# Kernel tuning notes

Hardware: AMD Instinct MI355X
Metric: run time of the kernel (lower is better)

The kernel has to match this reference:

```python
import jax, jax.numpy as jnp
import numpy as np

T, N, D, R, E = 512, 32, 300, 3, 64
NUM_NODES, VG = 70000, 40000


def setup_inputs() -> dict:
    key = jax.random.key(0)
    ks = jax.random.split(key, 10)
    return {
        "x_indices": jax.random.randint(ks[0], (T, N), 0, NUM_NODES),
        "edge_src": jax.random.randint(ks[1], (T, R, E), 0, N),
        "edge_dst": jax.random.randint(ks[2], (T, R, E), 0, N),
        "X": jax.random.normal(ks[3], (NUM_NODES, D), dtype=jnp.float32) * 0.1,
        "conv_W": jax.random.normal(ks[4], (R, D, D), dtype=jnp.float32) * 0.05,
        "W0": jax.random.normal(ks[5], (D, D), dtype=jnp.float32) * 0.05,
        "Wu": jax.random.normal(ks[6], (N * D, D), dtype=jnp.float32) * 0.01,
        "Uu": jax.random.normal(ks[7], (D, D), dtype=jnp.float32) * 0.05,
        "Wg": jax.random.normal(ks[8], (VG, D), dtype=jnp.float32) * 0.05,
        "bg": jnp.zeros((VG,), dtype=jnp.float32),
    }


def gcn_conv(x, W, src, dst):
    """torch_geometric GCNConv(bias=False): add self-loops, D^-1/2 (A+I) D^-1/2 (x W)."""
    n = x.shape[0]
    h = x @ W  # [N, D]
    loop = jnp.arange(n)
    s = jnp.concatenate([src, loop])
    t = jnp.concatenate([dst, loop])
    deg = jax.ops.segment_sum(jnp.ones_like(t, dtype=x.dtype), t, num_segments=n)
    dinv = jnp.where(deg > 0, jax.lax.rsqrt(jnp.maximum(deg, 1e-12)), 0.0)
    norm = dinv[s] * dinv[t]  # [E+N]
    return jax.ops.segment_sum(h[s] * norm[:, None], t, num_segments=n)


def reference(x_indices, edge_src, edge_dst, X, conv_W, W0, Wu, Uu, Wg, bg):
    def step(mem, inp):
        idx, src, dst = inp  # [N], [R,E], [R,E]
        x = X[idx]  # grapharea features [N, D]
        # sum of per-relation GCNConv outputs
        conv = jnp.sum(
            jax.vmap(gcn_conv, in_axes=(None, 0, 0, 0))(x, conv_W, src, dst), axis=0
        )
        proposed = conv + x @ W0  # eye(N) @ (x @ W0) == x @ W0
        # GRU-style update gate: [1, N*D] @ [N*D, D] + mem_row0 @ [D, D]
        gate = jax.nn.sigmoid(x.reshape(1, -1) @ Wu + mem[0:1] @ Uu)  # [1, D]
        new_mem = gate * proposed + (1.0 - gate) * mem  # broadcast over N rows
        logits = jnp.maximum(new_mem[0], 0.0) @ Wg.T + bg  # [VG]
        # memory is a non-grad buffer in torch (.data.copy_): stop gradient through time
        return jax.lax.stop_gradient(new_mem), jax.nn.log_softmax(logits)

    mem0 = jnp.zeros((N, D), dtype=X.dtype)
    _, log_probs = jax.lax.scan(step, mem0, (x_indices, edge_src, edge_dst))
    # include_senses=False: per-step torch.tensor(0) stacked -> zeros([T])
    return log_probs, jnp.zeros((x_indices.shape[0],), dtype=jnp.int32)
```

## Files before the change

kernel.cpp:

```cpp
#include <hip/hip_runtime.h>
#include <hip/hip_bf16.h>
#include <math.h>

#define T_ 512
#define N_ 32
#define D_ 300
#define R_ 3
#define E_ 64
#define VG_ 40000

typedef __attribute__((ext_vector_type(8))) short bf16x8;
typedef __attribute__((ext_vector_type(4))) float f32x4;

#define LGKM_BARRIER() asm volatile("s_waitcnt lgkmcnt(0)\n\ts_barrier" ::: "memory")

static __device__ inline unsigned short f2b(float f) {
  __hip_bfloat16 h = __float2bfloat16(f);
  return *(unsigned short*)&h;
}

__global__ void k_zero(float* __restrict__ p, int n) {
  int i = blockIdx.x * blockDim.x + threadIdx.x;
  if (i < n) p[i] = 0.f;
}

__global__ void k_tr_wu(const float* __restrict__ Wu, unsigned short* __restrict__ Wt) {
  __shared__ float s[32][33];
  int kb = blockIdx.x * 32, nb = blockIdx.y * 32;
  int tn = threadIdx.x & 31, tr = threadIdx.x >> 5;
  for (int i = tr; i < 32; i += 8) {
    int k = kb + i, n = nb + tn;
    s[i][tn] = (n < 300) ? Wu[(size_t)k * 300 + n] : 0.f;
  }
  __syncthreads();
  for (int i = tr; i < 32; i += 8) {
    int n = nb + i, k = kb + tn;
    Wt[(size_t)n * 9600 + k] = f2b(s[tn][i]);
  }
}

__global__ void k_tr_wcat(const float* __restrict__ convW, const float* __restrict__ W0,
                          unsigned short* __restrict__ Wt) {
  __shared__ float s[32][33];
  int kb = blockIdx.x * 32, nb = blockIdx.y * 32;
  int tn = threadIdx.x & 31, tr = threadIdx.x >> 5;
  for (int i = tr; i < 32; i += 8) {
    int k = kb + i, n = nb + tn;
    float v = 0.f;
    if (n < 300 && k < 1200)
      v = (k < 900) ? convW[(size_t)k * 300 + n] : W0[(size_t)(k - 900) * 300 + n];
    s[i][tn] = v;
  }
  __syncthreads();
  for (int i = tr; i < 32; i += 8) {
    int n = nb + i, k = kb + tn;
    Wt[(size_t)n * 1216 + k] = f2b(s[tn][i]);
  }
}

__global__ void k_gather(const int* __restrict__ xidx, const int* __restrict__ esrc,
                         const int* __restrict__ edst, const float* __restrict__ X,
                         unsigned short* __restrict__ xg, unsigned short* __restrict__ Ag)
{
  const int t = blockIdx.x;
  __shared__ int s_idx[N_];
  __shared__ int s_src[R_][E_];
  __shared__ int s_dst[R_][E_];
  __shared__ int s_deg[R_][N_];
  __shared__ float s_dinv[R_][N_];
  const int tid = threadIdx.x;

  if (tid < N_) s_idx[tid] = xidx[t * N_ + tid];
  if (tid < R_ * E_) {
    int r = tid / E_, e = tid % E_;
    s_src[r][e] = esrc[(t * R_ + r) * E_ + e];
    s_dst[r][e] = edst[(t * R_ + r) * E_ + e];
  }
  if (tid < R_ * N_) ((int*)s_deg)[tid] = 1;
  __syncthreads();
  if (tid < R_ * E_) {
    int r = tid / E_;
    atomicAdd(&s_deg[r][s_dst[r][tid % E_]], 1);
  }
  __syncthreads();
  if (tid < R_ * N_) ((float*)s_dinv)[tid] = rsqrtf((float)((int*)s_deg)[tid]);
  __syncthreads();

  for (int nd = tid; nd < N_ * D_; nd += blockDim.x) {
    int n = nd / D_, d = nd % D_;
    xg[(size_t)t * (N_ * D_) + nd] = f2b(X[(size_t)s_idx[n] * D_ + d]);
  }
  if (tid < D_) {
    int d = tid;
    float x0 = X[(size_t)s_idx[0] * D_ + d];
    #pragma unroll
    for (int r = 0; r < R_; ++r) {
      float dinv0 = s_dinv[r][0];
      float acc = dinv0 * dinv0 * x0;
      for (int e = 0; e < E_; ++e) {
        if (s_dst[r][e] == 0) {
          int s = s_src[r][e];
          acc += s_dinv[r][s] * dinv0 * X[(size_t)s_idx[s] * D_ + d];
        }
      }
      Ag[(size_t)t * 1216 + r * D_ + d] = f2b(acc);
    }
    Ag[(size_t)t * 1216 + 900 + d] = f2b(x0);
  }
  if (tid < 16) Ag[(size_t)t * 1216 + 1200 + tid] = 0;
}

template<bool ATOMIC>
__global__ __launch_bounds__(256) void k_bgemm(
    const unsigned short* __restrict__ A,
    const unsigned short* __restrict__ B,
    float* __restrict__ C, int ldc, int Ncols, int K, int kchunk)
{
  const int tid = threadIdx.x;
  const int wid = tid >> 6, lane = tid & 63;
  const int l16 = lane & 15, lq = lane >> 4;
  const int bm = blockIdx.x * 128 + (wid & 1) * 64;
  const int bn = blockIdx.y * 128 + (wid >> 1) * 64;
  const int k0 = blockIdx.z * kchunk;
  const int nk = kchunk / 32;

  f32x4 acc[4][4] = {};
  const unsigned short* ap[4];
  const unsigned short* bp[4];
  #pragma unroll
  for (int mt = 0; mt < 4; ++mt) ap[mt] = A + (size_t)(bm + mt * 16 + l16) * K + k0 + lq * 8;
  #pragma unroll
  for (int nt = 0; nt < 4; ++nt) bp[nt] = B + (size_t)(bn + nt * 16 + l16) * K + k0 + lq * 8;

  #pragma unroll 2
  for (int c = 0; c < nk; ++c) {
    bf16x8 af[4], bfr[4];
    #pragma unroll
    for (int mt = 0; mt < 4; ++mt) af[mt] = *(const bf16x8*)(ap[mt] + c * 32);
    #pragma unroll
    for (int nt = 0; nt < 4; ++nt) bfr[nt] = *(const bf16x8*)(bp[nt] + c * 32);
    #pragma unroll
    for (int mt = 0; mt < 4; ++mt)
      #pragma unroll
      for (int nt = 0; nt < 4; ++nt)
        acc[mt][nt] = __builtin_amdgcn_mfma_f32_16x16x32_bf16(af[mt], bfr[nt], acc[mt][nt], 0, 0, 0);
  }

  #pragma unroll
  for (int mt = 0; mt < 4; ++mt) {
    #pragma unroll
    for (int r = 0; r < 4; ++r) {
      int row = bm + mt * 16 + lq * 4 + r;
      #pragma unroll
      for (int nt = 0; nt < 4; ++nt) {
        int col = bn + nt * 16 + l16;
        if (col < Ncols) {
          if (ATOMIC) atomicAdd(&C[(size_t)row * ldc + col], acc[mt][nt][r]);
          else        C[(size_t)row * ldc + col] = acc[mt][nt][r];
        }
      }
    }
  }
}

__global__ __launch_bounds__(256, 2) void k_lgemm(
    const unsigned short* __restrict__ A, const float* __restrict__ Wg,
    const float* __restrict__ bg, float* __restrict__ C)
{
  const int tid = threadIdx.x;
  const int wid = tid >> 6, lane = tid & 63;
  const int l16 = lane & 15, lq = lane >> 4;
  const int bn = blockIdx.x * 64;
  const int m0 = wid * 128;

  f32x4 acc[8][4] = {};
  const unsigned short* ap[8];
  const float* bp[4];
  #pragma unroll
  for (int mt = 0; mt < 8; ++mt) ap[mt] = A + (size_t)(m0 + mt * 16 + l16) * 320 + lq * 8;
  #pragma unroll
  for (int nt = 0; nt < 4; ++nt) bp[nt] = Wg + (size_t)(bn + nt * 16 + l16) * 300;

  #pragma unroll
  for (int c = 0; c < 10; ++c) {
    bf16x8 bfr[4];
    if (c < 9) {
      #pragma unroll
      for (int nt = 0; nt < 4; ++nt) {
        f32x4 x = *(const f32x4*)(bp[nt] + c * 32 + lq * 8);
        f32x4 y = *(const f32x4*)(bp[nt] + c * 32 + lq * 8 + 4);
        bf16x8 bv;
        #pragma unroll
        for (int j = 0; j < 4; ++j) { bv[j] = (short)f2b(x[j]); bv[4 + j] = (short)f2b(y[j]); }
        bfr[nt] = bv;
      }
    } else {
      #pragma unroll
      for (int nt = 0; nt < 4; ++nt) {
        bf16x8 bv;
        #pragma unroll
        for (int j = 0; j < 8; ++j) {
          int k = 288 + lq * 8 + j;
          bv[j] = (short)((k < 300) ? f2b(bp[nt][k]) : 0);
        }
        bfr[nt] = bv;
      }
    }
    bf16x8 af[8];
    #pragma unroll
    for (int mt = 0; mt < 8; ++mt) af[mt] = *(const bf16x8*)(ap[mt] + c * 32);
    #pragma unroll
    for (int mt = 0; mt < 8; ++mt)
      #pragma unroll
      for (int nt = 0; nt < 4; ++nt)
        acc[mt][nt] = __builtin_amdgcn_mfma_f32_16x16x32_bf16(af[mt], bfr[nt], acc[mt][nt], 0, 0, 0);
  }

  float bb[4];
  #pragma unroll
  for (int nt = 0; nt < 4; ++nt) bb[nt] = bg[bn + nt * 16 + l16];
  #pragma unroll
  for (int mt = 0; mt < 8; ++mt) {
    #pragma unroll
    for (int r = 0; r < 4; ++r) {
      int row = m0 + mt * 16 + lq * 4 + r;
      #pragma unroll
      for (int nt = 0; nt < 4; ++nt) {
        int col = bn + nt * 16 + l16;
        C[(size_t)row * VG_ + col] = acc[mt][nt][r] + bb[nt];
      }
    }
  }
}

__global__ __launch_bounds__(640) void k_rec(
    const float* __restrict__ gx, const float* __restrict__ P0,
    const float* __restrict__ Uu, unsigned short* __restrict__ Mrelu_bf)
{
  __shared__ __align__(16) unsigned short m_bf[320];
  __shared__ float zs[320];
  __shared__ unsigned short mr_s[8 * 320];
  const int tid = threadIdx.x;
  const int wid = tid >> 6, lane = tid & 63;
  const int l16 = lane & 15, lq = lane >> 4;
  const int nt0 = wid * 2, nt1 = wid * 2 + 1;

  bf16x8 b0[10], b1[10];
  {
    int n0 = nt0 * 16 + l16, n1 = nt1 * 16 + l16;
    #pragma unroll
    for (int c = 0; c < 10; ++c) {
      bf16x8 v0, v1;
      #pragma unroll
      for (int j = 0; j < 8; ++j) {
        int k = c * 32 + lq * 8 + j;
        float f0 = (k < 300 && n0 < 300) ? Uu[(size_t)k * 300 + n0] : 0.f;
        float f1 = (k < 300 && n1 < 300) ? Uu[(size_t)k * 300 + n1] : 0.f;
        v0[j] = (short)f2b(f0);
        v1[j] = (short)f2b(f1);
      }
      b0[c] = v0; b1[c] = v1;
    }
  }

  float m_reg = 0.f;
  if (tid < 320) m_bf[tid] = 0;
  float gx_cur = 0.f, p0_cur = 0.f, gx_nxt = 0.f, p0_nxt = 0.f;
  if (tid < 300) { gx_cur = gx[tid]; p0_cur = P0[tid]; }
  __syncthreads();

  for (int t = 0; t < T_; ++t) {
    if (tid < 300 && t + 1 < T_) {
      gx_nxt = gx[(size_t)(t + 1) * D_ + tid];
      p0_nxt = P0[(size_t)(t + 1) * D_ + tid];
    }
    f32x4 acc0 = {0.f, 0.f, 0.f, 0.f}, acc1 = {0.f, 0.f, 0.f, 0.f};
    #pragma unroll
    for (int c = 0; c < 10; ++c) {
      bf16x8 a = *(const bf16x8*)(m_bf + c * 32 + lq * 8);
      acc0 = __builtin_amdgcn_mfma_f32_16x16x32_bf16(a, b0[c], acc0, 0, 0, 0);
      acc1 = __builtin_amdgcn_mfma_f32_16x16x32_bf16(a, b1[c], acc1, 0, 0, 0);
    }
    if (lq == 0) {
      zs[nt0 * 16 + l16] = acc0[0];
      zs[nt1 * 16 + l16] = acc1[0];
    }
    LGKM_BARRIER();
    if (tid < 300) {
      float z = zs[tid] + gx_cur;
      float g = 1.f / (1.f + __expf(-z));
      m_reg = fmaf(g, p0_cur - m_reg, m_reg);
      m_bf[tid] = f2b(m_reg);
      mr_s[(t & 7) * 320 + tid] = f2b(fmaxf(m_reg, 0.f));
    } else if (tid < 320) {
      mr_s[(t & 7) * 320 + tid] = 0;
    }
    LGKM_BARRIER();
    if ((t & 7) == 7) {
      unsigned int* dst = (unsigned int*)(Mrelu_bf + (size_t)(t - 7) * 320);
      const unsigned int* src = (const unsigned int*)mr_s;
      for (int w = tid; w < 1280; w += 640) dst[w] = src[w];
    }
    gx_cur = gx_nxt; p0_cur = p0_nxt;
  }
}

__global__ __launch_bounds__(256) void k_lsm(float* __restrict__ out) {
  const int t = blockIdx.x;
  float* row = out + (size_t)t * VG_;
  const f32x4* row4 = (const f32x4*)row;
  __shared__ float redM[256];
  __shared__ float redS[256];
  const int tid = threadIdx.x;
  float lm = -1e30f, ls = 0.f;
  for (int v = tid; v < VG_ / 4; v += 256) {
    f32x4 z4 = row4[v];
    #pragma unroll
    for (int j = 0; j < 4; ++j) {
      float z = z4[j];
      float m2 = fmaxf(lm, z);
      ls = ls * expf(lm - m2) + expf(z - m2);
      lm = m2;
    }
  }
  redM[tid] = lm; redS[tid] = ls;
  __syncthreads();
  for (int s = 128; s > 0; s >>= 1) {
    if (tid < s) {
      float mA = redM[tid], mB = redM[tid + s];
      float M = fmaxf(mA, mB);
      redS[tid] = redS[tid] * expf(mA - M) + redS[tid + s] * expf(mB - M);
      redM[tid] = M;
    }
    __syncthreads();
  }
  float lse = redM[0] + logf(redS[0]);
  f32x4* row4w = (f32x4*)row;
  for (int v = tid; v < VG_ / 4; v += 256) {
    f32x4 z4 = row4w[v];
    #pragma unroll
    for (int j = 0; j < 4; ++j) z4[j] -= lse;
    row4w[v] = z4;
  }
  if (tid == 0) out[(size_t)T_ * VG_ + t] = 0.0f;
}

extern "C" void kernel_launch(void* const* d_in, const int* in_sizes, int n_in,
                              void* d_out, int out_size, void* d_ws, size_t ws_size,
                              hipStream_t stream) {
  const int*   xidx  = (const int*)d_in[0];
  const int*   esrc  = (const int*)d_in[1];
  const int*   edst  = (const int*)d_in[2];
  const float* X     = (const float*)d_in[3];
  const float* convW = (const float*)d_in[4];
  const float* W0    = (const float*)d_in[5];
  const float* Wu    = (const float*)d_in[6];
  const float* Uu    = (const float*)d_in[7];
  const float* Wg    = (const float*)d_in[8];
  const float* bg    = (const float*)d_in[9];
  float* out = (float*)d_out;

  char* ws = (char*)d_ws;
  float*          gx     = (float*)ws;
  float*          P0     = (float*)(ws + 614400);
  unsigned short* MreluB = (unsigned short*)(ws + 1228800);
  unsigned short* xgB    = (unsigned short*)(ws + 1556480);
  unsigned short* AgB    = (unsigned short*)(ws + 11386880);
  unsigned short* WuT    = (unsigned short*)(ws + 12632064);
  unsigned short* WcatT  = (unsigned short*)(ws + 20004864);

  k_zero<<<(T_ * D_ + 255) / 256, 256, 0, stream>>>(gx, T_ * D_);
  k_tr_wu<<<dim3(300, 12), 256, 0, stream>>>(Wu, WuT);
  k_tr_wcat<<<dim3(38, 12), 256, 0, stream>>>(convW, W0, WcatT);
  k_gather<<<T_, 320, 0, stream>>>(xidx, esrc, edst, X, xgB, AgB);

  k_bgemm<true><<<dim3(4, 3, 10), 256, 0, stream>>>(xgB, WuT, gx, D_, D_, 9600, 960);
  k_bgemm<false><<<dim3(4, 3, 1), 256, 0, stream>>>(AgB, WcatT, P0, D_, D_, 1216, 1216);

  k_rec<<<1, 640, 0, stream>>>(gx, P0, Uu, MreluB);

  k_lgemm<<<dim3(625), 256, 0, stream>>>(MreluB, Wg, bg, out);
  k_lsm<<<T_, 256, 0, stream>>>(out);
}
```

Measured before the change: 891.3 us.

## Remove one barrier per step in recurrent gate kernel via double-buffered state

Each lane that owns a column now computes the sigmoid gate straight from its MFMA accumulator, so the shared-memory staging of z and one of the two barriers per timestep go away. The bf16 memory vector is double-buffered, and the relu staging ring is widened to 16 slots so the flush of 8 rows can overlap later writes. The MFMA chain is also split into two independent accumulators to shorten the dependency chain. The cost is that the gx/P0 prefetch now happens after use inside the step instead of ahead of the matmul, so its load latency may be exposed.

```diff
diff --git a/kernel.cpp b/kernel.cpp
--- a/kernel.cpp
+++ b/kernel.cpp
@@ -237,9 +237,8 @@
     const float* __restrict__ gx, const float* __restrict__ P0,
     const float* __restrict__ Uu, unsigned short* __restrict__ Mrelu_bf)
 {
-  __shared__ __align__(16) unsigned short m_bf[320];
-  __shared__ float zs[320];
-  __shared__ unsigned short mr_s[8 * 320];
+  __shared__ __align__(16) unsigned short m_bf[2][320];
+  __shared__ unsigned short mr_s[16 * 320];
   const int tid = threadIdx.x;
   const int wid = tid >> 6, lane = tid & 63;
   const int l16 = lane & 15, lq = lane >> 4;
@@ -263,45 +262,64 @@
     }
   }
 
-  float m_reg = 0.f;
-  if (tid < 320) m_bf[tid] = 0;
-  float gx_cur = 0.f, p0_cur = 0.f, gx_nxt = 0.f, p0_nxt = 0.f;
-  if (tid < 300) { gx_cur = gx[tid]; p0_cur = P0[tid]; }
+  const int c0 = wid * 32 + l16;
+  const int c1 = c0 + 16;
+  const bool gate = (lq == 0);
+  float m0 = 0.f, m1 = 0.f;
+  float gx0 = 0.f, gx1 = 0.f, p00 = 0.f, p01 = 0.f;
+  if (gate) {
+    if (c0 < 300) { gx0 = gx[c0]; p00 = P0[c0]; }
+    if (c1 < 300) { gx1 = gx[c1]; p01 = P0[c1]; }
+  }
+
+  if (tid < 320) { m_bf[0][tid] = 0; m_bf[1][tid] = 0; }
+  for (int i = tid; i < 16 * 320; i += 640) mr_s[i] = 0;
   __syncthreads();
 
   for (int t = 0; t < T_; ++t) {
-    if (tid < 300 && t + 1 < T_) {
-      gx_nxt = gx[(size_t)(t + 1) * D_ + tid];
-      p0_nxt = P0[(size_t)(t + 1) * D_ + tid];
-    }
-    f32x4 acc0 = {0.f, 0.f, 0.f, 0.f}, acc1 = {0.f, 0.f, 0.f, 0.f};
-    #pragma unroll
-    for (int c = 0; c < 10; ++c) {
-      bf16x8 a = *(const bf16x8*)(m_bf + c * 32 + lq * 8);
-      acc0 = __builtin_amdgcn_mfma_f32_16x16x32_bf16(a, b0[c], acc0, 0, 0, 0);
-      acc1 = __builtin_amdgcn_mfma_f32_16x16x32_bf16(a, b1[c], acc1, 0, 0, 0);
-    }
-    if (lq == 0) {
-      zs[nt0 * 16 + l16] = acc0[0];
-      zs[nt1 * 16 + l16] = acc1[0];
-    }
-    LGKM_BARRIER();
-    if (tid < 300) {
-      float z = zs[tid] + gx_cur;
-      float g = 1.f / (1.f + __expf(-z));
-      m_reg = fmaf(g, p0_cur - m_reg, m_reg);
-      m_bf[tid] = f2b(m_reg);
-      mr_s[(t & 7) * 320 + tid] = f2b(fmaxf(m_reg, 0.f));
-    } else if (tid < 320) {
-      mr_s[(t & 7) * 320 + tid] = 0;
+    const int rb = t & 1, wb = rb ^ 1;
+    bf16x8 a[10];
+    #pragma unroll
+    for (int c = 0; c < 10; ++c)
+      a[c] = *(const bf16x8*)(&m_bf[rb][c * 32 + lq * 8]);
+    f32x4 A0 = {0.f,0.f,0.f,0.f}, A1 = {0.f,0.f,0.f,0.f};
+    f32x4 B0 = {0.f,0.f,0.f,0.f}, B1 = {0.f,0.f,0.f,0.f};
+    #pragma unroll
+    for (int cc = 0; cc < 5; ++cc) {
+      A0 = __builtin_amdgcn_mfma_f32_16x16x32_bf16(a[cc],     b0[cc],     A0, 0, 0, 0);
+      A1 = __builtin_amdgcn_mfma_f32_16x16x32_bf16(a[cc],     b1[cc],     A1, 0, 0, 0);
+      B0 = __builtin_amdgcn_mfma_f32_16x16x32_bf16(a[cc + 5], b0[cc + 5], B0, 0, 0, 0);
+      B1 = __builtin_amdgcn_mfma_f32_16x16x32_bf16(a[cc + 5], b1[cc + 5], B1, 0, 0, 0);
+    }
+    if (gate) {
+      const int slot = (t & 15) * 320;
+      if (c0 < 300) {
+        float z = A0[0] + B0[0] + gx0;
+        float g = __frcp_rn(1.f + __expf(-z));
+        m0 = fmaf(g, p00 - m0, m0);
+        m_bf[wb][c0] = f2b(m0);
+        mr_s[slot + c0] = f2b(fmaxf(m0, 0.f));
+      }
+      if (c1 < 300) {
+        float z = A1[0] + B1[0] + gx1;
+        float g = __frcp_rn(1.f + __expf(-z));
+        m1 = fmaf(g, p01 - m1, m1);
+        m_bf[wb][c1] = f2b(m1);
+        mr_s[slot + c1] = f2b(fmaxf(m1, 0.f));
+      }
+      if (t + 1 < T_) {
+        const size_t o = (size_t)(t + 1) * D_;
+        if (c0 < 300) { gx0 = gx[o + c0]; p00 = P0[o + c0]; }
+        if (c1 < 300) { gx1 = gx[o + c1]; p01 = P0[o + c1]; }
+      }
     }
     LGKM_BARRIER();
     if ((t & 7) == 7) {
-      unsigned int* dst = (unsigned int*)(Mrelu_bf + (size_t)(t - 7) * 320);
-      const unsigned int* src = (const unsigned int*)mr_s;
+      const int base = t - 7;
+      const unsigned int* src = (const unsigned int*)(mr_s + (base & 15) * 320);
+      unsigned int* dst = (unsigned int*)(Mrelu_bf + (size_t)base * 320);
       for (int w = tid; w < 1280; w += 640) dst[w] = src[w];
     }
-    gx_cur = gx_nxt; p0_cur = p0_nxt;
   }
 }
 
```

Measured after the change: 889.5 us. About the same (-0.2%).
